# Optimization experiments

Measured on AMD Instinct MI355X. Metric: run time of the kernel, lower is better.

## Reference

```python
import math
import jax, jax.numpy as jnp
import numpy as np


def _procrustes_R(H):
    # H: [B, 3, 3]. Rotation R = V @ U^T with reflection fix (det(R) >= 0),
    # matching torch.svd convention (v = V, not V^T).
    u, s, vh = jnp.linalg.svd(H)
    v = jnp.swapaxes(vh, -1, -2)                       # [B,3,3]
    r = jnp.einsum('bij,bkj->bik', v, u)               # V @ U^T
    det = jnp.linalg.det(r)                            # [B]
    sign = jnp.where(det < 0, -1.0, 1.0)               # flip last column of V (reflect = diag(1,1,-1))
    flip = jnp.stack([jnp.ones_like(sign), jnp.ones_like(sign), sign], axis=-1)[:, None, :]
    v = v * flip
    return jnp.einsum('bij,bkj->bik', v, u)


def setup_inputs() -> dict:
    key = jax.random.key(0)
    k1, k2, k3, k4 = jax.random.split(key, 4)
    B, D, N, M = 8, 512, 2048, 2048
    return {
        'src_embedding': jax.random.normal(k1, (B, D, N), dtype=jnp.float32),
        'tgt_embedding': jax.random.normal(k2, (B, D, M), dtype=jnp.float32),
        'src': jax.random.normal(k3, (B, 3, N), dtype=jnp.float32),
        'tgt': jax.random.normal(k4, (B, 3, M), dtype=jnp.float32),
    }


def reference(src_embedding, tgt_embedding, src, tgt):
    d_k = src_embedding.shape[1]
    # attention correspondence: scores[b,n,m]
    scores = jnp.einsum('bdn,bdm->bnm', src_embedding, tgt_embedding) / math.sqrt(d_k)
    scores = jax.nn.softmax(scores, axis=2)
    # soft correspondence of src points in tgt: [B,3,N]
    src_corr = jnp.einsum('bdm,bnm->bdn', tgt, scores)
    src_mean = src.mean(axis=2, keepdims=True)          # [B,3,1]
    src_centered = src - src_mean
    src_corr_centered = src_corr - src_corr.mean(axis=2, keepdims=True)
    H = jnp.einsum('bin,bjn->bij', src_centered, src_corr_centered)  # [B,3,3]
    R = _procrustes_R(H)
    t = jnp.einsum('bij,bjk->bik', -R, src_mean) + tgt.mean(axis=2, keepdims=True)
    return R, t.reshape(src.shape[0], 3)
```

## Files before the change

kernel.cpp:

```cpp
#include <hip/hip_runtime.h>
#include <hip/hip_bf16.h>

#define BQ 8
#define DIM 512
#define NN 2048
#define MM 2048
#define MSPLIT 16

typedef __attribute__((ext_vector_type(8))) short short8;
typedef __attribute__((ext_vector_type(8))) unsigned short ushort8;
typedef __attribute__((ext_vector_type(4))) float floatx4;

#define GLOAD_LDS(gp, lp) \
    __builtin_amdgcn_global_load_lds( \
        (const __attribute__((address_space(1))) void*)(gp), \
        (__attribute__((address_space(3))) void*)(lp), 16, 0, 0)


static __device__ __forceinline__ unsigned short f2bf(float x) {
    __hip_bfloat16 h = __float2bfloat16(x);
    return *(unsigned short*)&h;
}

__global__ __launch_bounds__(256) void transpose_cast_kernel(
    const float* __restrict__ src_emb,
    const float* __restrict__ tgt_emb,
    __hip_bfloat16* __restrict__ Abf,
    __hip_bfloat16* __restrict__ Bbf)
{
    const int n0 = blockIdx.x * 64;
    const int d0 = blockIdx.y * 64;
    const int b  = blockIdx.z & 7;
    const int which = blockIdx.z >> 3;

    const float* in = (which == 0 ? src_emb : tgt_emb) + (size_t)b * DIM * NN;
    __hip_bfloat16* out = (which == 0 ? Abf : Bbf) + (size_t)b * NN * DIM;

    __shared__ float tl[64][65];

    const int t = threadIdx.x;

    {
        const int u = t & 15;
        const int r = t >> 4;
        #pragma unroll
        for (int rr = r; rr < 64; rr += 16) {
            float4 v = *(const float4*)&in[(size_t)(d0 + rr) * NN + n0 + u * 4];
            tl[rr][u * 4 + 0] = v.x;
            tl[rr][u * 4 + 1] = v.y;
            tl[rr][u * 4 + 2] = v.z;
            tl[rr][u * 4 + 3] = v.w;
        }
    }
    __syncthreads();

    {
        const int u = t & 7;
        const int r = t >> 3;
        #pragma unroll
        for (int rn = r; rn < 64; rn += 32) {
            ushort8 o;
            #pragma unroll
            for (int j = 0; j < 8; j++)
                o[j] = f2bf(tl[u * 8 + j][rn]);
            *(ushort8*)&out[(size_t)(n0 + rn) * DIM + d0 + u * 8] = o;
        }
    }
}

__global__ __launch_bounds__(512, 2) void attn_mfma_kernel(
    const __hip_bfloat16* __restrict__ Abf,
    const __hip_bfloat16* __restrict__ Bbf,
    const float* __restrict__ tgt,
    float* __restrict__ part)
{
    const int nt = blockIdx.x;
    const int qt = blockIdx.y;
    const int b  = blockIdx.z;
    const int t  = threadIdx.x;
    const int wave = t >> 6;
    const int lane = t & 63;
    const int lm   = lane & 15;
    const int quad = lane >> 4;
    const int wn   = wave * 32;
    const int bw   = wave * 16;

    __shared__ short As[256 * 64];
    __shared__ short Bs[128 * 64];

    const __hip_bfloat16* Abase = Abf + ((size_t)(b * NN + nt * 256)) * DIM;
    const int m0 = qt * 128;
    const __hip_bfloat16* Bbase = Bbf + ((size_t)(b * MM + m0)) * DIM;
    const float* Tb = tgt + (size_t)b * 3 * MM;

    const float SCALE = 0.044194173824159216f * 1.4426950408889634f;

    const int r8 = lane >> 3;
    const int c8 = lane & 7;
    const int cc = c8 ^ r8;
    const __hip_bfloat16* gA = Abase + (size_t)(wn + r8) * DIM + cc * 8;
    const __hip_bfloat16* gB = Bbase + (size_t)(bw + r8) * DIM + cc * 8;
    short* lA = &As[wn * 64];
    short* lB = &Bs[bw * 64];

    floatx4 acc[2][8];
    #pragma unroll
    for (int i = 0; i < 2; i++)
        #pragma unroll
        for (int j = 0; j < 8; j++)
            acc[i][j] = (floatx4){0.f, 0.f, 0.f, 0.f};

    #pragma unroll
    for (int kt = 0; kt < 8; kt++) {
        #pragma unroll
        for (int i = 0; i < 4; i++)
            GLOAD_LDS(gA + kt * 64 + (size_t)i * 8 * DIM, lA + i * 512);
        #pragma unroll
        for (int i = 0; i < 2; i++)
            GLOAD_LDS(gB + kt * 64 + (size_t)i * 8 * DIM, lB + i * 512);
        __syncthreads();

        #pragma unroll
        for (int ks = 0; ks < 2; ks++) {
            const int pc = (((ks * 4 + quad) ^ (lane & 7)) * 8);
            short8 af0 = *(const short8*)&As[(wn +      lm) * 64 + pc];
            short8 af1 = *(const short8*)&As[(wn + 16 + lm) * 64 + pc];
            #pragma unroll
            for (int j = 0; j < 8; j++) {
                short8 bf = *(const short8*)&Bs[(j * 16 + lm) * 64 + pc];
                acc[0][j] = __builtin_amdgcn_mfma_f32_16x16x32_bf16(af0, bf, acc[0][j], 0, 0, 0);
                acc[1][j] = __builtin_amdgcn_mfma_f32_16x16x32_bf16(af1, bf, acc[1][j], 0, 0, 0);
            }
        }
        __syncthreads();
    }

    float v0[8], v1[8], v2[8];
    #pragma unroll
    for (int j = 0; j < 8; j++) {
        int vc = m0 + j * 16 + lm;
        v0[j] = Tb[vc];
        v1[j] = Tb[MM + vc];
        v2[j] = Tb[2 * MM + vc];
    }

    const size_t slot = (size_t)(b * MSPLIT + qt) * NN;
    #pragma unroll
    for (int i = 0; i < 2; i++) {
        float l4[4] = {0,0,0,0};
        float o0[4] = {0,0,0,0};
        float o1[4] = {0,0,0,0};
        float o2[4] = {0,0,0,0};
        #pragma unroll
        for (int j = 0; j < 8; j++) {
            #pragma unroll
            for (int r = 0; r < 4; r++) {
                float e = __builtin_amdgcn_exp2f(acc[i][j][r] * SCALE);
                l4[r] += e;
                o0[r] += e * v0[j];
                o1[r] += e * v1[j];
                o2[r] += e * v2[j];
            }
        }
        #pragma unroll
        for (int m = 1; m <= 8; m <<= 1) {
            #pragma unroll
            for (int r = 0; r < 4; r++) {
                l4[r] += __shfl_xor(l4[r], m);
                o0[r] += __shfl_xor(o0[r], m);
                o1[r] += __shfl_xor(o1[r], m);
                o2[r] += __shfl_xor(o2[r], m);
            }
        }
        if (lm == 0) {
            #pragma unroll
            for (int r = 0; r < 4; r++) {
                int n = nt * 256 + wn + i * 16 + quad * 4 + r;
                ((float4*)part)[slot + n] = make_float4(l4[r], o0[r], o1[r], o2[r]);
            }
        }
    }
}

__global__ __launch_bounds__(128) void reduce1_kernel(
    const float* __restrict__ part,
    const float* __restrict__ src,
    const float* __restrict__ tgt,
    float* __restrict__ red)
{
    const int chunk = blockIdx.x;
    const int b     = blockIdx.y;
    const int t     = threadIdx.x;
    const int n     = chunk * 128 + t;

    const float4* w4 = (const float4*)part;
    const float* S = src + (size_t)b * 3 * NN;
    const float* T = tgt + (size_t)b * 3 * MM;

    float l = 0.f, y0 = 0.f, y1 = 0.f, y2 = 0.f;
    #pragma unroll
    for (int q = 0; q < 16; q++) {
        float4 p = w4[(size_t)(b * 16 + q) * NN + n];
        l += p.x; y0 += p.y; y1 += p.z; y2 += p.w;
    }
    float inv = 1.0f / l;
    float c0 = y0 * inv, c1 = y1 * inv, c2 = y2 * inv;
    float s0 = S[n], s1 = S[NN + n], s2 = S[2 * NN + n];

    float vals[18];
    vals[0] = s0;  vals[1] = s1;  vals[2] = s2;
    vals[3] = c0;  vals[4] = c1;  vals[5] = c2;
    vals[6] = T[n]; vals[7] = T[MM + n]; vals[8] = T[2 * MM + n];
    vals[9]  = s0 * c0; vals[10] = s0 * c1; vals[11] = s0 * c2;
    vals[12] = s1 * c0; vals[13] = s1 * c1; vals[14] = s1 * c2;
    vals[15] = s2 * c0; vals[16] = s2 * c1; vals[17] = s2 * c2;

    #pragma unroll
    for (int m = 1; m <= 32; m <<= 1)
        #pragma unroll
        for (int c = 0; c < 18; c++)
            vals[c] += __shfl_xor(vals[c], m);

    __shared__ float w0[18];
    if (t == 64)
        #pragma unroll
        for (int c = 0; c < 18; c++) w0[c] = vals[c];
    __syncthreads();
    if (t == 0)
        #pragma unroll
        for (int c = 0; c < 18; c++)
            red[(size_t)(b * 16 + chunk) * 18 + c] = vals[c] + w0[c];
}

__global__ __launch_bounds__(64) void procrustes_kernel(
    const float* __restrict__ red,
    float* __restrict__ out)
{
    const int b = blockIdx.x;
    const int t = threadIdx.x;

    __shared__ float res[18];
    if (t < 18) {
        float a = 0.f;
        #pragma unroll
        for (int q = 0; q < 16; q++)
            a += red[(size_t)(b * 16 + q) * 18 + t];
        res[t] = a;
    }
    __syncthreads();

    if (t == 0) {
        const float invN = 1.0f / (float)NN;
        float mus[3], muc[3], mut[3], H[3][3];
        for (int i = 0; i < 3; i++) {
            mus[i] = res[i] * invN;
            muc[i] = res[3 + i] * invN;
            mut[i] = res[6 + i] * invN;
        }
        for (int i = 0; i < 3; i++)
            for (int j = 0; j < 3; j++)
                H[i][j] = res[9 + i * 3 + j] - (float)NN * mus[i] * muc[j];

        float A[3][3];
        for (int i = 0; i < 3; i++)
            for (int j = 0; j < 3; j++)
                A[i][j] = H[0][i] * H[0][j] + H[1][i] * H[1][j] + H[2][i] * H[2][j];

        float V[3][3] = {{1,0,0},{0,1,0},{0,0,1}};
        for (int sweep = 0; sweep < 6; sweep++) {
            for (int pi = 0; pi < 3; pi++) {
                int p = (pi < 2) ? 0 : 1;
                int q = (pi == 0) ? 1 : 2;
                float apq = A[p][q];
                if (fabsf(apq) < 1e-30f) continue;
                float tau = (A[q][q] - A[p][p]) / (2.0f * apq);
                float tt = (tau >= 0.0f) ? 1.0f / (tau + sqrtf(1.0f + tau * tau))
                                         : -1.0f / (-tau + sqrtf(1.0f + tau * tau));
                float c = 1.0f / sqrtf(1.0f + tt * tt);
                float s = tt * c;
                for (int k = 0; k < 3; k++) {
                    float akp = A[k][p], akq = A[k][q];
                    A[k][p] = c * akp - s * akq;
                    A[k][q] = s * akp + c * akq;
                }
                for (int k = 0; k < 3; k++) {
                    float apk = A[p][k], aqk = A[q][k];
                    A[p][k] = c * apk - s * aqk;
                    A[q][k] = s * apk + c * aqk;
                }
                for (int k = 0; k < 3; k++) {
                    float vkp = V[k][p], vkq = V[k][q];
                    V[k][p] = c * vkp - s * vkq;
                    V[k][q] = s * vkp + c * vkq;
                }
            }
        }

        float lam[3] = {A[0][0], A[1][1], A[2][2]};
        int idx[3] = {0, 1, 2};
        for (int a = 0; a < 2; a++)
            for (int bb = 0; bb < 2 - a; bb++)
                if (lam[idx[bb]] < lam[idx[bb + 1]]) { int tmp = idx[bb]; idx[bb] = idx[bb + 1]; idx[bb + 1] = tmp; }

        float Vc[3][3], U[3][3];
        for (int c = 0; c < 3; c++) {
            float sv = sqrtf(fmaxf(lam[idx[c]], 0.0f));
            float isv = 1.0f / fmaxf(sv, 1e-20f);
            for (int r = 0; r < 3; r++) {
                Vc[r][c] = V[r][idx[c]];
                U[r][c] = (H[r][0] * V[0][idx[c]] + H[r][1] * V[1][idx[c]] + H[r][2] * V[2][idx[c]]) * isv;
            }
        }

        {
            float nrm = rsqrtf(U[0][0]*U[0][0] + U[1][0]*U[1][0] + U[2][0]*U[2][0]);
            for (int r = 0; r < 3; r++) U[r][0] *= nrm;
            float d01 = U[0][0]*U[0][1] + U[1][0]*U[1][1] + U[2][0]*U[2][1];
            for (int r = 0; r < 3; r++) U[r][1] -= d01 * U[r][0];
            nrm = rsqrtf(U[0][1]*U[0][1] + U[1][1]*U[1][1] + U[2][1]*U[2][1]);
            for (int r = 0; r < 3; r++) U[r][1] *= nrm;
            float d02 = U[0][0]*U[0][2] + U[1][0]*U[1][2] + U[2][0]*U[2][2];
            float d12 = U[0][1]*U[0][2] + U[1][1]*U[1][2] + U[2][1]*U[2][2];
            for (int r = 0; r < 3; r++) U[r][2] -= d02 * U[r][0] + d12 * U[r][1];
            nrm = rsqrtf(U[0][2]*U[0][2] + U[1][2]*U[1][2] + U[2][2]*U[2][2]);
            for (int r = 0; r < 3; r++) U[r][2] *= nrm;
        }

        float det = H[0][0]*(H[1][1]*H[2][2] - H[1][2]*H[2][1])
                  - H[0][1]*(H[1][0]*H[2][2] - H[1][2]*H[2][0])
                  + H[0][2]*(H[1][0]*H[2][1] - H[1][1]*H[2][0]);
        float sgn = (det < 0.0f) ? -1.0f : 1.0f;

        float R[3][3];
        for (int i = 0; i < 3; i++)
            for (int j = 0; j < 3; j++)
                R[i][j] = Vc[i][0]*U[j][0] + Vc[i][1]*U[j][1] + sgn * Vc[i][2]*U[j][2];

        for (int i = 0; i < 3; i++)
            for (int j = 0; j < 3; j++)
                out[b * 9 + i * 3 + j] = R[i][j];
        for (int i = 0; i < 3; i++)
            out[BQ * 9 + b * 3 + i] = mut[i] - (R[i][0]*mus[0] + R[i][1]*mus[1] + R[i][2]*mus[2]);
    }
}

extern "C" void kernel_launch(void* const* d_in, const int* in_sizes, int n_in,
                              void* d_out, int out_size, void* d_ws, size_t ws_size,
                              hipStream_t stream) {
    const float* src_emb = (const float*)d_in[0];
    const float* tgt_emb = (const float*)d_in[1];
    const float* src     = (const float*)d_in[2];
    const float* tgt     = (const float*)d_in[3];
    float* out = (float*)d_out;

    float* part = (float*)d_ws;
    __hip_bfloat16* Abf = (__hip_bfloat16*)((char*)d_ws + (4 << 20));
    __hip_bfloat16* Bbf = (__hip_bfloat16*)((char*)d_ws + (20 << 20));
    float* red = (float*)((char*)d_ws + (36 << 20));

    dim3 gridT(NN / 64, DIM / 64, 2 * BQ);
    transpose_cast_kernel<<<gridT, 256, 0, stream>>>(src_emb, tgt_emb, Abf, Bbf);

    dim3 gridA(NN / 256, MSPLIT, BQ);
    attn_mfma_kernel<<<gridA, 512, 0, stream>>>(Abf, Bbf, tgt, part);

    dim3 gridR(16, BQ);
    reduce1_kernel<<<gridR, 128, 0, stream>>>(part, src, tgt, red);

    procrustes_kernel<<<BQ, 64, 0, stream>>>(red, out);
}
```

Baseline: 169.0 us.

## Fuse reduction and Procrustes kernels into one head kernel; hoist tgt loads

Merges the two tail kernels (per-chunk reduction and the Procrustes SVD) into a single 1024-thread block per batch. Each block reduces all 2048 points itself and then runs the solve, which removes one launch and the intermediate workspace round-trip. Separately, the tgt value loads in the attention kernel are moved before the GEMM loop so their latency overlaps the MFMA work. The cost is higher register pressure in the attention kernel and only 8 blocks for the head reduction, so that phase runs with less parallelism.

New measurement: 172.3 us. About the same (+2.0%).

```diff
diff --git a/kernel.cpp b/kernel.cpp
--- a/kernel.cpp
+++ b/kernel.cpp
@@ -95,6 +95,15 @@
 
     const float SCALE = 0.044194173824159216f * 1.4426950408889634f;
 
+    float v0[8], v1[8], v2[8];
+    #pragma unroll
+    for (int j = 0; j < 8; j++) {
+        int vc = m0 + j * 16 + lm;
+        v0[j] = Tb[vc];
+        v1[j] = Tb[MM + vc];
+        v2[j] = Tb[2 * MM + vc];
+    }
+
     const int r8 = lane >> 3;
     const int c8 = lane & 7;
     const int cc = c8 ^ r8;
@@ -135,15 +144,6 @@
         __syncthreads();
     }
 
-    float v0[8], v1[8], v2[8];
-    #pragma unroll
-    for (int j = 0; j < 8; j++) {
-        int vc = m0 + j * 16 + lm;
-        v0[j] = Tb[vc];
-        v1[j] = Tb[MM + vc];
-        v2[j] = Tb[2 * MM + vc];
-    }
-
     const size_t slot = (size_t)(b * MSPLIT + qt) * NN;
     #pragma unroll
     for (int i = 0; i < 2; i++) {
@@ -182,74 +182,66 @@
     }
 }
 
-__global__ __launch_bounds__(128) void reduce1_kernel(
+__global__ __launch_bounds__(1024) void head_kernel(
     const float* __restrict__ part,
     const float* __restrict__ src,
     const float* __restrict__ tgt,
-    float* __restrict__ red)
-{
-    const int chunk = blockIdx.x;
-    const int b     = blockIdx.y;
-    const int t     = threadIdx.x;
-    const int n     = chunk * 128 + t;
-
-    const float4* w4 = (const float4*)part;
-    const float* S = src + (size_t)b * 3 * NN;
-    const float* T = tgt + (size_t)b * 3 * MM;
-
-    float l = 0.f, y0 = 0.f, y1 = 0.f, y2 = 0.f;
-    #pragma unroll
-    for (int q = 0; q < 16; q++) {
-        float4 p = w4[(size_t)(b * 16 + q) * NN + n];
-        l += p.x; y0 += p.y; y1 += p.z; y2 += p.w;
-    }
-    float inv = 1.0f / l;
-    float c0 = y0 * inv, c1 = y1 * inv, c2 = y2 * inv;
-    float s0 = S[n], s1 = S[NN + n], s2 = S[2 * NN + n];
-
-    float vals[18];
-    vals[0] = s0;  vals[1] = s1;  vals[2] = s2;
-    vals[3] = c0;  vals[4] = c1;  vals[5] = c2;
-    vals[6] = T[n]; vals[7] = T[MM + n]; vals[8] = T[2 * MM + n];
-    vals[9]  = s0 * c0; vals[10] = s0 * c1; vals[11] = s0 * c2;
-    vals[12] = s1 * c0; vals[13] = s1 * c1; vals[14] = s1 * c2;
-    vals[15] = s2 * c0; vals[16] = s2 * c1; vals[17] = s2 * c2;
-
-    #pragma unroll
-    for (int m = 1; m <= 32; m <<= 1)
-        #pragma unroll
-        for (int c = 0; c < 18; c++)
-            vals[c] += __shfl_xor(vals[c], m);
-
-    __shared__ float w0[18];
-    if (t == 64)
-        #pragma unroll
-        for (int c = 0; c < 18; c++) w0[c] = vals[c];
-    __syncthreads();
-    if (t == 0)
-        #pragma unroll
-        for (int c = 0; c < 18; c++)
-            red[(size_t)(b * 16 + chunk) * 18 + c] = vals[c] + w0[c];
-}
-
-__global__ __launch_bounds__(64) void procrustes_kernel(
-    const float* __restrict__ red,
     float* __restrict__ out)
 {
     const int b = blockIdx.x;
     const int t = threadIdx.x;
 
-    __shared__ float res[18];
-    if (t < 18) {
-        float a = 0.f;
-        #pragma unroll
-        for (int q = 0; q < 16; q++)
-            a += red[(size_t)(b * 16 + q) * 18 + t];
-        res[t] = a;
-    }
+    const float4* w4 = (const float4*)part;
+    const float* S = src + (size_t)b * 3 * NN;
+    const float* T = tgt + (size_t)b * 3 * MM;
+
+    float vals[18];
+    #pragma unroll
+    for (int c = 0; c < 18; c++) vals[c] = 0.f;
+
+    #pragma unroll
+    for (int h = 0; h < 2; h++) {
+        const int n = h * 1024 + t;
+        float l = 0.f, y0 = 0.f, y1 = 0.f, y2 = 0.f;
+        #pragma unroll
+        for (int q = 0; q < 16; q++) {
+            float4 p = w4[(size_t)(b * 16 + q) * NN + n];
+            l += p.x; y0 += p.y; y1 += p.z; y2 += p.w;
+        }
+        float inv = 1.0f / l;
+        float c0 = y0 * inv, c1 = y1 * inv, c2 = y2 * inv;
+        float s0 = S[n], s1 = S[NN + n], s2 = S[2 * NN + n];
+        vals[0] += s0;  vals[1] += s1;  vals[2] += s2;
+        vals[3] += c0;  vals[4] += c1;  vals[5] += c2;
+        vals[6] += T[n]; vals[7] += T[MM + n]; vals[8] += T[2 * MM + n];
+        vals[9]  += s0 * c0; vals[10] += s0 * c1; vals[11] += s0 * c2;
+        vals[12] += s1 * c0; vals[13] += s1 * c1; vals[14] += s1 * c2;
+        vals[15] += s2 * c0; vals[16] += s2 * c1; vals[17] += s2 * c2;
+    }
+
+    #pragma unroll
+    for (int m = 1; m <= 32; m <<= 1)
+        #pragma unroll
+        for (int c = 0; c < 18; c++)
+            vals[c] += __shfl_xor(vals[c], m);
+
+    __shared__ float warr[16][18];
+    const int wave = t >> 6;
+    if ((t & 63) == 0)
+        #pragma unroll
+        for (int c = 0; c < 18; c++) warr[wave][c] = vals[c];
     __syncthreads();
 
     if (t == 0) {
+        float res[18];
+        #pragma unroll
+        for (int c = 0; c < 18; c++) {
+            float a = 0.f;
+            #pragma unroll
+            for (int w = 0; w < 16; w++) a += warr[w][c];
+            res[c] = a;
+        }
+
         const float invN = 1.0f / (float)NN;
         float mus[3], muc[3], mut[3], H[3][3];
         for (int i = 0; i < 3; i++) {
@@ -356,7 +348,6 @@
     float* part = (float*)d_ws;
     __hip_bfloat16* Abf = (__hip_bfloat16*)((char*)d_ws + (4 << 20));
     __hip_bfloat16* Bbf = (__hip_bfloat16*)((char*)d_ws + (20 << 20));
-    float* red = (float*)((char*)d_ws + (36 << 20));
 
     dim3 gridT(NN / 64, DIM / 64, 2 * BQ);
     transpose_cast_kernel<<<gridT, 256, 0, stream>>>(src_emb, tgt_emb, Abf, Bbf);
@@ -364,8 +355,5 @@
     dim3 gridA(NN / 256, MSPLIT, BQ);
     attn_mfma_kernel<<<gridA, 512, 0, stream>>>(Abf, Bbf, tgt, part);
 
-    dim3 gridR(16, BQ);
-    reduce1_kernel<<<gridR, 128, 0, stream>>>(part, src, tgt, red);
-
-    procrustes_kernel<<<BQ, 64, 0, stream>>>(red, out);
-}
+    head_kernel<<<BQ, 1024, 0, stream>>>(part, src, tgt, out);
+}
```
